# Kernel tuning notes

Hardware: AMD Instinct MI355X
Metric: run time of the kernel (lower is better)

The kernel has to match this reference:

```python
import jax, jax.numpy as jnp
import numpy as np

B, T, H, NH, L, V, FF = 2, 1024, 1024, 16, 6, 8192, 4096
D = H // NH
EPS = 1e-5


def _ln(x, g, b):
    mu = jnp.mean(x, axis=-1, keepdims=True)
    var = jnp.mean(jnp.square(x - mu), axis=-1, keepdims=True)
    return (x - mu) * jax.lax.rsqrt(var + EPS) * g + b


def setup_inputs() -> dict:
    key = jax.random.key(0)
    ks = jax.random.split(key, 12)
    s = 1.0 / np.sqrt(H)
    return {
        "x": jax.random.randint(ks[0], (B, T), 0, V),
        "tok_emb": jax.random.normal(ks[1], (V, H), jnp.float32) * s,
        "pos_emb": jax.random.normal(ks[2], (1, T, H), jnp.float32) * s,
        "Wq": jax.random.normal(ks[3], (L, H, H), jnp.float32) * s,
        "bq": jnp.zeros((L, H), jnp.float32),
        "Wk": jax.random.normal(ks[4], (L, H, H), jnp.float32) * s,
        "bk": jnp.zeros((L, H), jnp.float32),
        "Wv": jax.random.normal(ks[5], (L, H, H), jnp.float32) * s,
        "bv": jnp.zeros((L, H), jnp.float32),
        "Wo": jax.random.normal(ks[6], (L, H, H), jnp.float32) * s,
        "bo": jnp.zeros((L, H), jnp.float32),
        "W1": jax.random.normal(ks[7], (L, H, FF), jnp.float32) * s,
        "b1": jnp.zeros((L, FF), jnp.float32),
        "W2": jax.random.normal(ks[8], (L, FF, H), jnp.float32) * (1.0 / np.sqrt(FF)),
        "b2": jnp.zeros((L, H), jnp.float32),
        "ln1_g": jnp.ones((L, H), jnp.float32),
        "ln1_b": jnp.zeros((L, H), jnp.float32),
        "ln2_g": jnp.ones((L, H), jnp.float32),
        "ln2_b": jnp.zeros((L, H), jnp.float32),
        "lnf_g": jnp.ones((H,), jnp.float32),
        "lnf_b": jnp.zeros((H,), jnp.float32),
        "headW": jax.random.normal(ks[9], (H, V), jnp.float32) * s,
        "headb": jnp.zeros((V,), jnp.float32),
    }


def _transformer(x, tok_emb, pos_emb, Wq, bq, Wk, bk, Wv, bv, Wo, bo,
                 W1, b1, W2, b2, ln1_g, ln1_b, ln2_g, ln2_b, lnf_g, lnf_b,
                 headW, headb):
    Tcur = x.shape[1]
    h = tok_emb[x] + pos_emb[:, :Tcur, :]            # [B,T,H]
    mask = jnp.tril(jnp.ones((Tcur, Tcur), bool))    # causal [T,T]
    scale = 1.0 / np.sqrt(D)

    def block(h, p):
        (wq, q_b, wk, k_b, wv, v_b, wo, o_b,
         w1, b1_, w2, b2_, g1, be1, g2, be2) = p
        q = (h @ wq + q_b).reshape(B, Tcur, NH, D)
        k = (h @ wk + k_b).reshape(B, Tcur, NH, D)
        v = (h @ wv + v_b).reshape(B, Tcur, NH, D)
        att = jnp.einsum('bqnd,bknd->bnqk', q, k) * scale
        att = jnp.where(mask, att, -jnp.inf)
        w = jax.nn.softmax(att, axis=-1)
        o = jnp.einsum('bnqk,bknd->bqnd', w, v).reshape(B, Tcur, H)
        h = _ln(h + (o @ wo + o_b), g1, be1)          # post-LN after attention
        m = jax.nn.gelu(h @ w1 + b1_, approximate=False) @ w2 + b2_
        h = _ln(h + m, g2, be2)                       # post-LN after MLP
        return h, None

    params = (Wq, bq, Wk, bk, Wv, bv, Wo, bo, W1, b1, W2, b2,
              ln1_g, ln1_b, ln2_g, ln2_b)
    h, _ = jax.lax.scan(block, h, params)
    h = _ln(h, lnf_g, lnf_b)
    return h @ headW + headb                          # [B,T,V]


def reference(x, tok_emb, pos_emb, Wq, bq, Wk, bk, Wv, bv, Wo, bo,
              W1, b1, W2, b2, ln1_g, ln1_b, ln2_g, ln2_b, lnf_g, lnf_b,
              headW, headb):
    return _transformer(x, tok_emb, pos_emb, Wq, bq, Wk, bk, Wv, bv, Wo, bo,
                        W1, b1, W2, b2, ln1_g, ln1_b, ln2_g, ln2_b,
                        lnf_g, lnf_b, headW, headb)
```

## Files before the change

### kernel.cpp

```cpp
#include <hip/hip_runtime.h>
#include <hip/hip_bf16.h>

#define DEV __device__ __forceinline__

typedef unsigned short u16;
typedef __attribute__((ext_vector_type(8))) short bf16x8;
typedef __attribute__((ext_vector_type(4))) float f32x4;

static constexpr int MB_ = 2;
static constexpr int T_  = 1024;
static constexpr int H_  = 1024;
static constexpr int NH_ = 16;
static constexpr int L_  = 6;
static constexpr int V_  = 8192;
static constexpr int FF_ = 4096;
static constexpr int M_  = MB_ * T_;
static constexpr int QKVN = 3 * H_;

DEV u16 f2bf(float x) {
  __hip_bfloat16 h = __float2bfloat16(x);
  return *reinterpret_cast<u16*>(&h);
}

__global__ __launch_bounds__(256) void embed_kernel(
    const int* __restrict__ x, const float* __restrict__ tok,
    const float* __restrict__ pos, float* __restrict__ h, u16* __restrict__ hb)
{
  int i = blockIdx.x;
  int t = threadIdx.x;
  int id = x[i];
  int tt = i & (T_ - 1);
  float4 a = *(const float4*)(tok + (size_t)id * H_ + t * 4);
  float4 b = *(const float4*)(pos + (size_t)tt * H_ + t * 4);
  float4 r = make_float4(a.x + b.x, a.y + b.y, a.z + b.z, a.w + b.w);
  *(float4*)(h + (size_t)i * H_ + t * 4) = r;
  ushort4 u = make_ushort4(f2bf(r.x), f2bf(r.y), f2bf(r.z), f2bf(r.w));
  *(ushort4*)(hb + (size_t)i * H_ + t * 4) = u;
}

DEV void transpose_tile128(const float* __restrict__ W, u16* __restrict__ WT,
                           int R, int C, int bx, int by)
{
  __shared__ float Ts[64][65];
  const int t = threadIdx.x;
  const int lr = t >> 4;
  const int lcq = (t & 15) * 4;
  #pragma unroll
  for (int si = 0; si < 2; ++si) {
    #pragma unroll
    for (int sj = 0; sj < 2; ++sj) {
      const int r0 = by * 128 + si * 64, c0 = bx * 128 + sj * 64;
      #pragma unroll
      for (int it = 0; it < 4; ++it) {
        int r = it * 16 + lr;
        float4 v = *(const float4*)(W + (size_t)(r0 + r) * C + c0 + lcq);
        Ts[r][lcq + 0] = v.x; Ts[r][lcq + 1] = v.y;
        Ts[r][lcq + 2] = v.z; Ts[r][lcq + 3] = v.w;
      }
      __syncthreads();
      #pragma unroll
      for (int it = 0; it < 4; ++it) {
        int n = it * 16 + lr;
        ushort4 u = make_ushort4(f2bf(Ts[lcq + 0][n]), f2bf(Ts[lcq + 1][n]),
                                 f2bf(Ts[lcq + 2][n]), f2bf(Ts[lcq + 3][n]));
        *(ushort4*)(WT + (size_t)(c0 + n) * R + r0 + lcq) = u;
      }
      __syncthreads();
    }
  }
}

__global__ __launch_bounds__(256) void transpose_layer_k(
    const float* __restrict__ Wq, const float* __restrict__ Wk,
    const float* __restrict__ Wv, const float* __restrict__ Wo,
    const float* __restrict__ W1, const float* __restrict__ W2,
    u16* qkvT, u16* oT, u16* w1T, u16* w2T)
{
  int t = blockIdx.x;
  if (t < 256) {
    int m = t >> 6, idx = t & 63, bx = idx & 7, by = idx >> 3;
    const float* W = (m == 0) ? Wq : (m == 1) ? Wk : (m == 2) ? Wv : Wo;
    u16* WT = (m == 3) ? oT : qkvT + (size_t)m * H_ * H_;
    transpose_tile128(W, WT, H_, H_, bx, by);
  } else if (t < 512) {
    int idx = t - 256;
    transpose_tile128(W1, w1T, H_, FF_, idx & 31, idx >> 5);
  } else {
    int idx = t - 512;
    transpose_tile128(W2, w2T, FF_, H_, idx & 7, idx >> 3);
  }
}

__global__ __launch_bounds__(256) void transpose_head_k(
    const float* __restrict__ hW, u16* __restrict__ hT)
{
  int idx = blockIdx.x;
  transpose_tile128(hW, hT, H_, V_, idx & 63, idx >> 6);
}

__global__ __launch_bounds__(256) void concat_qkv_bias(
    const float* __restrict__ bq, const float* __restrict__ bk,
    const float* __restrict__ bv, float* __restrict__ outb)
{
  int l = blockIdx.x;
  for (int j = threadIdx.x; j < H_; j += 256) {
    outb[(size_t)l * QKVN + j]          = bq[(size_t)l * H_ + j];
    outb[(size_t)l * QKVN + H_ + j]     = bk[(size_t)l * H_ + j];
    outb[(size_t)l * QKVN + 2 * H_ + j] = bv[(size_t)l * H_ + j];
  }
}


#define GLOAD_LDS16(g, l)                                              \
  __builtin_amdgcn_global_load_lds(                                    \
      (const __attribute__((address_space(1))) void*)(g),              \
      (__attribute__((address_space(3))) void*)(l), 16, 0, 0)

DEV void stage_t(const u16* __restrict__ G, int ldk, int r0g, int kofs,
                 u16* lds, int w, int lane)
{
  const int rl = ((lane >> 3) << 1) | ((lane >> 2) & 1);
  #pragma unroll
  for (int j = 0; j < 2; ++j) {
    const int row0 = w * 32 + j * 16;
    const int row = row0 + rl;
    const int c = (lane & 3) ^ (((row0 >> 1) + (lane >> 3)) & 3);
    const u16* g = G + (size_t)(r0g + row) * ldk + kofs + c * 8;
    GLOAD_LDS16(g, lds + row0 * 32);
  }
}

DEV bf16x8 frag3(const u16* lds, int rr, int ch) {
  return *(const bf16x8*)(lds + (rr >> 1) * 64 + (rr & 1) * 32 +
                          ((ch ^ ((rr >> 1) & 3)) * 8));
}

template<int N>
DEV void wait_vm_barrier() {
  asm volatile("s_waitcnt vmcnt(%0)" :: "n"(N) : "memory");
  __builtin_amdgcn_s_barrier();
}

DEV void comp3(const u16* As, const u16* Bs, f32x4 (&acc)[4][4],
               int wr, int wc, int lc, int lg)
{
  bf16x8 af[4], bv[4];
  #pragma unroll
  for (int mi = 0; mi < 4; ++mi)
    af[mi] = frag3(As, wr * 64 + mi * 16 + lc, lg);
  #pragma unroll
  for (int ni = 0; ni < 4; ++ni)
    bv[ni] = frag3(Bs, wc * 64 + ni * 16 + lc, lg);
  #pragma unroll
  for (int mi = 0; mi < 4; ++mi)
    #pragma unroll
    for (int ni = 0; ni < 4; ++ni)
      acc[mi][ni] = __builtin_amdgcn_mfma_f32_16x16x32_bf16(af[mi], bv[ni], acc[mi][ni], 0, 0, 0);
}

template<bool PARTIAL, bool DO_GELU, bool WF, bool WB>
__global__ __launch_bounds__(256, 2) void gemm3(
    const u16* __restrict__ A, const u16* __restrict__ BT,
    const float* __restrict__ bias, float* __restrict__ Cf,
    u16* __restrict__ Cb, float* __restrict__ P, int N, int K, int Ksub)
{
  __shared__ __align__(16) u16 As[4][128][32];
  __shared__ __align__(16) u16 Bs[4][128][32];

  const int tid = threadIdx.x;
  const int lane = tid & 63, w = tid >> 6;
  const int wr = w >> 1, wc = w & 1;
  const int lc = lane & 15, lg = lane >> 4;

  const int gx = gridDim.x, gy = gridDim.y;
  const int nwg = gx * gy;
  const int lid = blockIdx.y * gx + blockIdx.x;
  const int q8 = nwg >> 3, r8s = nwg & 7;
  const int xcd = lid & 7, ord = lid >> 3;
  const int sid = (xcd < r8s ? xcd * (q8 + 1) : r8s * (q8 + 1) + (xcd - r8s) * q8) + ord;
  const int m0 = (sid % gy) * 128, n0 = (sid / gy) * 128;

  const int kb = blockIdx.z * Ksub;
  const int NT = Ksub >> 5;

  f32x4 acc[4][4];
  #pragma unroll
  for (int i = 0; i < 4; ++i)
    #pragma unroll
    for (int j = 0; j < 4; ++j) {
      f32x4 z = {0.f, 0.f, 0.f, 0.f};
      acc[i][j] = z;
    }

  auto STG = [&](int t, int b) {
    stage_t(A,  K, m0, kb + t * 32, &As[b][0][0], w, lane);
    stage_t(BT, K, n0, kb + t * 32, &Bs[b][0][0], w, lane);
  };

  STG(0, 0);
  STG(1, 1);
  int t = 0;
  for (; t < NT - 2; ++t) {
    STG(t + 2, (t + 2) & 3);
    wait_vm_barrier<8>();
    comp3(&As[t & 3][0][0], &Bs[t & 3][0][0], acc, wr, wc, lc, lg);
  }
  wait_vm_barrier<4>();
  comp3(&As[t & 3][0][0], &Bs[t & 3][0][0], acc, wr, wc, lc, lg);
  ++t;
  wait_vm_barrier<0>();
  comp3(&As[t & 3][0][0], &Bs[t & 3][0][0], acc, wr, wc, lc, lg);

  const size_t zofs = (size_t)blockIdx.z * M_ * N;
  #pragma unroll
  for (int mi = 0; mi < 4; ++mi) {
    #pragma unroll
    for (int ni = 0; ni < 4; ++ni) {
      int gn = n0 + wc * 64 + ni * 16 + lc;
      float bvv = PARTIAL ? 0.f : bias[gn];
      #pragma unroll
      for (int r = 0; r < 4; ++r) {
        int gm = m0 + wr * 64 + mi * 16 + lg * 4 + r;
        float v = acc[mi][ni][r];
        if (PARTIAL) {
          P[zofs + (size_t)gm * N + gn] = v;
        } else {
          v += bvv;
          if (DO_GELU) v = 0.5f * v * (1.f + erff(v * 0.70710678118654752f));
          if (WF) Cf[(size_t)gm * N + gn] = v;
          if (WB) Cb[(size_t)gm * N + gn] = f2bf(v);
        }
      }
    }
  }
}

__global__ __launch_bounds__(256) void ln_kernel(
    const float* __restrict__ X,
    const float* __restrict__ g, const float* __restrict__ be,
    u16* __restrict__ Hb)
{
  __shared__ float red[8];
  int row = blockIdx.x, t = threadIdx.x;
  int lane = t & 63, w = t >> 6;
  float4 v = *(const float4*)(X + (size_t)row * H_ + t * 4);
  float s = v.x + v.y + v.z + v.w;
  float q = v.x * v.x + v.y * v.y + v.z * v.z + v.w * v.w;
  #pragma unroll
  for (int o = 1; o < 64; o <<= 1) { s += __shfl_xor(s, o); q += __shfl_xor(q, o); }
  if (lane == 0) { red[w] = s; red[4 + w] = q; }
  __syncthreads();
  float S = red[0] + red[1] + red[2] + red[3];
  float Q = red[4] + red[5] + red[6] + red[7];
  float mu  = S * (1.f / H_);
  float var = Q * (1.f / H_) - mu * mu;
  float inv = rsqrtf(var + 1e-5f);
  float4 gv = *(const float4*)(g  + t * 4);
  float4 bv = *(const float4*)(be + t * 4);
  ushort4 u = make_ushort4(f2bf((v.x - mu) * inv * gv.x + bv.x),
                           f2bf((v.y - mu) * inv * gv.y + bv.y),
                           f2bf((v.z - mu) * inv * gv.z + bv.z),
                           f2bf((v.w - mu) * inv * gv.w + bv.w));
  *(ushort4*)(Hb + (size_t)row * H_ + t * 4) = u;
}

__global__ __launch_bounds__(256) void ln2_kernel(
    const float* __restrict__ P, int S,
    const float* __restrict__ bias,
    const float* __restrict__ g, const float* __restrict__ be,
    float* __restrict__ h, u16* __restrict__ hb)
{
  __shared__ float red[8];
  int row = blockIdx.x, t = threadIdx.x;
  int lane = t & 63, w = t >> 6;
  float4 v = *(const float4*)(h + (size_t)row * H_ + t * 4);
  float4 bb = *(const float4*)(bias + t * 4);
  v.x += bb.x; v.y += bb.y; v.z += bb.z; v.w += bb.w;
  for (int s0 = 0; s0 < S; ++s0) {
    float4 p = *(const float4*)(P + (size_t)s0 * M_ * H_ + (size_t)row * H_ + t * 4);
    v.x += p.x; v.y += p.y; v.z += p.z; v.w += p.w;
  }
  float s = v.x + v.y + v.z + v.w;
  float q = v.x * v.x + v.y * v.y + v.z * v.z + v.w * v.w;
  #pragma unroll
  for (int o = 1; o < 64; o <<= 1) { s += __shfl_xor(s, o); q += __shfl_xor(q, o); }
  if (lane == 0) { red[w] = s; red[4 + w] = q; }
  __syncthreads();
  float S1 = red[0] + red[1] + red[2] + red[3];
  float Q1 = red[4] + red[5] + red[6] + red[7];
  float mu  = S1 * (1.f / H_);
  float var = Q1 * (1.f / H_) - mu * mu;
  float inv = rsqrtf(var + 1e-5f);
  float4 gv = *(const float4*)(g  + t * 4);
  float4 bv = *(const float4*)(be + t * 4);
  float o0 = (v.x - mu) * inv * gv.x + bv.x;
  float o1 = (v.y - mu) * inv * gv.y + bv.y;
  float o2 = (v.z - mu) * inv * gv.z + bv.z;
  float o3 = (v.w - mu) * inv * gv.w + bv.w;
  *(float4*)(h + (size_t)row * H_ + t * 4) = make_float4(o0, o1, o2, o3);
  ushort4 u = make_ushort4(f2bf(o0), f2bf(o1), f2bf(o2), f2bf(o3));
  *(ushort4*)(hb + (size_t)row * H_ + t * 4) = u;
}

__global__ __launch_bounds__(256) void attn_kernel(
    const u16* __restrict__ qkv, u16* __restrict__ Og)
{
  __shared__ __align__(16) u16 Ks[2][64][72];
  __shared__ __align__(16) u16 Vs[2][64][72];
  __shared__ __align__(16) u16 QPs[4][16][72];

  const int qb = gridDim.x - 1 - blockIdx.x;
  const int bh = blockIdx.y;
  const int b = bh >> 4, hh = bh & 15;
  const int q0 = qb * 64;
  const size_t base  = ((size_t)b * T_) * QKVN + (size_t)hh * 64;
  const size_t baseO = ((size_t)b * T_) * H_ + (size_t)hh * 64;

  const int tid = threadIdx.x;
  const int lane = tid & 63, w = tid >> 6;
  const int lc = lane & 15, lg = lane >> 4;

  const int r8 = tid >> 3, d8 = (tid & 7) << 3;
  const int vk = tid & 31, vd = (tid >> 5) << 3;

  u16* Qflat = &QPs[0][0][0];

  bf16x8 kr[2], vr[2];
  #pragma unroll
  for (int i = 0; i < 2; ++i) {
    kr[i] = *(const bf16x8*)(qkv + base + H_ + (size_t)(i * 32 + r8) * QKVN + d8);
    vr[i] = *(const bf16x8*)(qkv + base + 2 * H_ + (size_t)(i * 32 + vk) * QKVN + vd);
  }
  #pragma unroll
  for (int i = 0; i < 2; ++i)
    *(bf16x8*)(Qflat + (size_t)(i * 32 + r8) * 72 + d8) =
      *(const bf16x8*)(qkv + base + (size_t)(q0 + i * 32 + r8) * QKVN + d8);
  #pragma unroll
  for (int i = 0; i < 2; ++i) {
    *(bf16x8*)&Ks[0][i * 32 + r8][d8] = kr[i];
    #pragma unroll
    for (int j = 0; j < 8; ++j) Vs[0][vd + j][i * 32 + vk] = ((const u16*)&vr[i])[j];
  }
  __syncthreads();
  bf16x8 aq0 = *(const bf16x8*)(Qflat + (size_t)(w * 16 + lc) * 72 + lg * 8);
  bf16x8 aq1 = *(const bf16x8*)(Qflat + (size_t)(w * 16 + lc) * 72 + 32 + lg * 8);

  float m_r[4], l_r[4];
  f32x4 oa[4];
  #pragma unroll
  for (int i = 0; i < 4; ++i) {
    m_r[i] = -1e30f; l_r[i] = 0.f;
    f32x4 z = {0.f, 0.f, 0.f, 0.f};
    oa[i] = z;
  }
  const float sc2 = 0.125f * 1.4426950408889634f;

  for (int kv = 0; kv <= qb; ++kv) {
    const int cur = kv & 1, nxt = cur ^ 1;
    if (kv < qb) {
      #pragma unroll
      for (int i = 0; i < 2; ++i) {
        kr[i] = *(const bf16x8*)(qkv + base + H_ + (size_t)((kv + 1) * 64 + i * 32 + r8) * QKVN + d8);
        vr[i] = *(const bf16x8*)(qkv + base + 2 * H_ + (size_t)((kv + 1) * 64 + i * 32 + vk) * QKVN + vd);
      }
    }

    f32x4 sfr[4];
    #pragma unroll
    for (int ni = 0; ni < 4; ++ni) { f32x4 z = {0.f,0.f,0.f,0.f}; sfr[ni] = z; }
    #pragma unroll
    for (int ni = 0; ni < 4; ++ni) {
      bf16x8 bk0 = *(const bf16x8*)&Ks[cur][ni * 16 + lc][lg * 8];
      bf16x8 bk1 = *(const bf16x8*)&Ks[cur][ni * 16 + lc][32 + lg * 8];
      sfr[ni] = __builtin_amdgcn_mfma_f32_16x16x32_bf16(aq0, bk0, sfr[ni], 0, 0, 0);
      sfr[ni] = __builtin_amdgcn_mfma_f32_16x16x32_bf16(aq1, bk1, sfr[ni], 0, 0, 0);
    }
    if (kv == qb) {
      #pragma unroll
      for (int ni = 0; ni < 4; ++ni)
        #pragma unroll
        for (int r = 0; r < 4; ++r)
          if (ni * 16 + lc > w * 16 + lg * 4 + r) sfr[ni][r] = -1e30f;
    }
    #pragma unroll
    for (int r = 0; r < 4; ++r) {
      float pm = fmaxf(fmaxf(sfr[0][r], sfr[1][r]), fmaxf(sfr[2][r], sfr[3][r]));
      pm = fmaxf(pm, __shfl_xor(pm, 1));
      pm = fmaxf(pm, __shfl_xor(pm, 2));
      pm = fmaxf(pm, __shfl_xor(pm, 4));
      pm = fmaxf(pm, __shfl_xor(pm, 8));
      float mn = fmaxf(m_r[r], pm);
      float al = exp2f(sc2 * (m_r[r] - mn));
      m_r[r] = mn; l_r[r] *= al;
      #pragma unroll
      for (int f = 0; f < 4; ++f) oa[f][r] *= al;
      float rs = 0.f;
      #pragma unroll
      for (int ni = 0; ni < 4; ++ni) {
        float p = exp2f(sc2 * (sfr[ni][r] - mn));
        sfr[ni][r] = p; rs += p;
      }
      rs += __shfl_xor(rs, 1); rs += __shfl_xor(rs, 2);
      rs += __shfl_xor(rs, 4); rs += __shfl_xor(rs, 8);
      l_r[r] += rs;
    }
    #pragma unroll
    for (int ni = 0; ni < 4; ++ni)
      #pragma unroll
      for (int r = 0; r < 4; ++r)
        QPs[w][lg * 4 + r][ni * 16 + lc] = f2bf(sfr[ni][r]);
    bf16x8 ap0 = *(const bf16x8*)&QPs[w][lc][lg * 8];
    bf16x8 ap1 = *(const bf16x8*)&QPs[w][lc][32 + lg * 8];
    #pragma unroll
    for (int f = 0; f < 4; ++f) {
      bf16x8 bv0 = *(const bf16x8*)&Vs[cur][f * 16 + lc][lg * 8];
      bf16x8 bv1 = *(const bf16x8*)&Vs[cur][f * 16 + lc][32 + lg * 8];
      oa[f] = __builtin_amdgcn_mfma_f32_16x16x32_bf16(ap0, bv0, oa[f], 0, 0, 0);
      oa[f] = __builtin_amdgcn_mfma_f32_16x16x32_bf16(ap1, bv1, oa[f], 0, 0, 0);
    }

    if (kv < qb) {
      #pragma unroll
      for (int i = 0; i < 2; ++i) {
        *(bf16x8*)&Ks[nxt][i * 32 + r8][d8] = kr[i];
        #pragma unroll
        for (int j = 0; j < 8; ++j) Vs[nxt][vd + j][i * 32 + vk] = ((const u16*)&vr[i])[j];
      }
      __syncthreads();
    }
  }

  #pragma unroll
  for (int r = 0; r < 4; ++r) {
    float inv = 1.f / l_r[r];
    int grow = q0 + w * 16 + lg * 4 + r;
    #pragma unroll
    for (int f = 0; f < 4; ++f)
      Og[baseO + (size_t)grow * H_ + f * 16 + lc] = f2bf(oa[f][r] * inv);
  }
}

extern "C" void kernel_launch(void* const* d_in, const int* in_sizes, int n_in,
                              void* d_out, int out_size, void* d_ws, size_t ws_size,
                              hipStream_t stream)
{
  const int*   x    = (const int*)  d_in[0];
  const float* tok  = (const float*)d_in[1];
  const float* pos  = (const float*)d_in[2];
  const float* Wq   = (const float*)d_in[3];
  const float* bq   = (const float*)d_in[4];
  const float* Wk   = (const float*)d_in[5];
  const float* bk   = (const float*)d_in[6];
  const float* Wv   = (const float*)d_in[7];
  const float* bv   = (const float*)d_in[8];
  const float* Wo   = (const float*)d_in[9];
  const float* bo   = (const float*)d_in[10];
  const float* W1   = (const float*)d_in[11];
  const float* b1   = (const float*)d_in[12];
  const float* W2   = (const float*)d_in[13];
  const float* b2   = (const float*)d_in[14];
  const float* g1   = (const float*)d_in[15];
  const float* be1  = (const float*)d_in[16];
  const float* g2   = (const float*)d_in[17];
  const float* be2  = (const float*)d_in[18];
  const float* gf   = (const float*)d_in[19];
  const float* bef  = (const float*)d_in[20];
  const float* hW   = (const float*)d_in[21];
  const float* hbias= (const float*)d_in[22];
  float* out = (float*)d_out;

  char* wsp = (char*)d_ws;
  size_t off = 0;
  auto alloc = [&](size_t bytes) -> void* {
    void* p = wsp + off;
    off += (bytes + 255) & ~(size_t)255;
    return p;
  };
  float* h    = (float*)alloc((size_t)M_ * H_ * 4);
  u16*   hb   = (u16*)  alloc((size_t)M_ * H_ * 2);
  u16*   qkv  = (u16*)  alloc((size_t)M_ * QKVN * 2);
  u16*   ob_  = (u16*)  alloc((size_t)M_ * H_ * 2);
  u16*   m1   = (u16*)  alloc((size_t)M_ * FF_ * 2);
  float* P    = (float*)alloc((size_t)4 * M_ * H_ * 4);
  u16*   hT   = (u16*)P;
  u16*   qkvT = (u16*)  alloc((size_t)QKVN * H_ * 2);
  u16*   oT   = (u16*)  alloc((size_t)H_ * H_ * 2);
  u16*   w1T  = (u16*)  alloc((size_t)H_ * FF_ * 2);
  u16*   w2T  = (u16*)  alloc((size_t)FF_ * H_ * 2);
  float* bqkv = (float*)alloc((size_t)L_ * QKVN * 4);
  (void)in_sizes; (void)n_in; (void)out_size; (void)ws_size;

  embed_kernel<<<M_, 256, 0, stream>>>(x, tok, pos, h, hb);
  concat_qkv_bias<<<L_, 256, 0, stream>>>(bq, bk, bv, bqkv);

  for (int l = 0; l < L_; ++l) {
    transpose_layer_k<<<768, 256, 0, stream>>>(
        Wq + (size_t)l * H_ * H_, Wk + (size_t)l * H_ * H_,
        Wv + (size_t)l * H_ * H_, Wo + (size_t)l * H_ * H_,
        W1 + (size_t)l * H_ * FF_, W2 + (size_t)l * FF_ * H_,
        qkvT, oT, w1T, w2T);
    gemm3<false, false, false, true><<<dim3(QKVN / 128, M_ / 128, 1), 256, 0, stream>>>(
        hb, qkvT, bqkv + (size_t)l * QKVN, nullptr, qkv, nullptr, QKVN, H_, H_);
    attn_kernel<<<dim3(T_ / 64, MB_ * NH_), 256, 0, stream>>>(qkv, ob_);
    gemm3<true, false, false, false><<<dim3(H_ / 128, M_ / 128, 2), 256, 0, stream>>>(
        ob_, oT, nullptr, nullptr, nullptr, P, H_, H_, H_ / 2);
    ln2_kernel<<<M_, 256, 0, stream>>>(P, 2, bo + l * H_, g1 + l * H_, be1 + l * H_, h, hb);
    gemm3<false, true, false, true><<<dim3(FF_ / 128, M_ / 128, 1), 256, 0, stream>>>(
        hb, w1T, b1 + (size_t)l * FF_, nullptr, m1, nullptr, FF_, H_, H_);
    gemm3<true, false, false, false><<<dim3(H_ / 128, M_ / 128, 4), 256, 0, stream>>>(
        m1, w2T, nullptr, nullptr, nullptr, P, H_, FF_, FF_ / 4);
    ln2_kernel<<<M_, 256, 0, stream>>>(P, 4, b2 + l * H_, g2 + l * H_, be2 + l * H_, h, hb);
  }

  ln_kernel<<<M_, 256, 0, stream>>>(h, gf, bef, hb);
  transpose_head_k<<<512, 256, 0, stream>>>(hW, hT);
  gemm3<false, false, true, false><<<dim3(V_ / 128, M_ / 128, 1), 256, 0, stream>>>(
      hb, hT, hbias, out, nullptr, nullptr, V_, H_, H_);
}
```

Before: 1.109 ms.

## Overlap next-layer weight transposes with W1 GEMM in a fused launch

```diff
diff --git a/kernel.cpp b/kernel.cpp
--- a/kernel.cpp
+++ b/kernel.cpp
@@ -22,26 +22,36 @@
   return *reinterpret_cast<u16*>(&h);
 }
 
-__global__ __launch_bounds__(256) void embed_kernel(
+__global__ __launch_bounds__(256) void embed_concat_kernel(
     const int* __restrict__ x, const float* __restrict__ tok,
-    const float* __restrict__ pos, float* __restrict__ h, u16* __restrict__ hb)
+    const float* __restrict__ pos, float* __restrict__ h, u16* __restrict__ hb,
+    const float* __restrict__ bq, const float* __restrict__ bk,
+    const float* __restrict__ bv, float* __restrict__ outb)
 {
   int i = blockIdx.x;
-  int t = threadIdx.x;
-  int id = x[i];
-  int tt = i & (T_ - 1);
-  float4 a = *(const float4*)(tok + (size_t)id * H_ + t * 4);
-  float4 b = *(const float4*)(pos + (size_t)tt * H_ + t * 4);
-  float4 r = make_float4(a.x + b.x, a.y + b.y, a.z + b.z, a.w + b.w);
-  *(float4*)(h + (size_t)i * H_ + t * 4) = r;
-  ushort4 u = make_ushort4(f2bf(r.x), f2bf(r.y), f2bf(r.z), f2bf(r.w));
-  *(ushort4*)(hb + (size_t)i * H_ + t * 4) = u;
-}
-
-DEV void transpose_tile128(const float* __restrict__ W, u16* __restrict__ WT,
-                           int R, int C, int bx, int by)
-{
-  __shared__ float Ts[64][65];
+  if (i < M_) {
+    int t = threadIdx.x;
+    int id = x[i];
+    int tt = i & (T_ - 1);
+    float4 a = *(const float4*)(tok + (size_t)id * H_ + t * 4);
+    float4 b = *(const float4*)(pos + (size_t)tt * H_ + t * 4);
+    float4 r = make_float4(a.x + b.x, a.y + b.y, a.z + b.z, a.w + b.w);
+    *(float4*)(h + (size_t)i * H_ + t * 4) = r;
+    ushort4 u = make_ushort4(f2bf(r.x), f2bf(r.y), f2bf(r.z), f2bf(r.w));
+    *(ushort4*)(hb + (size_t)i * H_ + t * 4) = u;
+  } else {
+    int l = i - M_;
+    for (int j = threadIdx.x; j < H_; j += 256) {
+      outb[(size_t)l * QKVN + j]          = bq[(size_t)l * H_ + j];
+      outb[(size_t)l * QKVN + H_ + j]     = bk[(size_t)l * H_ + j];
+      outb[(size_t)l * QKVN + 2 * H_ + j] = bv[(size_t)l * H_ + j];
+    }
+  }
+}
+
+DEV void transpose_tile128s(float (*Ts)[65], const float* __restrict__ W,
+                            u16* __restrict__ WT, int R, int C, int bx, int by)
+{
   const int t = threadIdx.x;
   const int lr = t >> 4;
   const int lcq = (t & 15) * 4;
@@ -70,44 +80,33 @@
   }
 }
 
+DEV void transpose_layer_body(float (*Ts)[65], int t,
+    const float* Wq, const float* Wk, const float* Wv, const float* Wo,
+    const float* W1, const float* W2,
+    u16* qkvT, u16* oT, u16* w1T, u16* w2T)
+{
+  if (t < 256) {
+    int m = t >> 6, idx = t & 63, bx = idx & 7, by = idx >> 3;
+    const float* W = (m == 0) ? Wq : (m == 1) ? Wk : (m == 2) ? Wv : Wo;
+    u16* WT = (m == 3) ? oT : qkvT + (size_t)m * H_ * H_;
+    transpose_tile128s(Ts, W, WT, H_, H_, bx, by);
+  } else if (t < 512) {
+    int idx = t - 256;
+    transpose_tile128s(Ts, W1, w1T, H_, FF_, idx & 31, idx >> 5);
+  } else {
+    int idx = t - 512;
+    transpose_tile128s(Ts, W2, w2T, FF_, H_, idx & 7, idx >> 3);
+  }
+}
+
 __global__ __launch_bounds__(256) void transpose_layer_k(
     const float* __restrict__ Wq, const float* __restrict__ Wk,
     const float* __restrict__ Wv, const float* __restrict__ Wo,
     const float* __restrict__ W1, const float* __restrict__ W2,
     u16* qkvT, u16* oT, u16* w1T, u16* w2T)
 {
-  int t = blockIdx.x;
-  if (t < 256) {
-    int m = t >> 6, idx = t & 63, bx = idx & 7, by = idx >> 3;
-    const float* W = (m == 0) ? Wq : (m == 1) ? Wk : (m == 2) ? Wv : Wo;
-    u16* WT = (m == 3) ? oT : qkvT + (size_t)m * H_ * H_;
-    transpose_tile128(W, WT, H_, H_, bx, by);
-  } else if (t < 512) {
-    int idx = t - 256;
-    transpose_tile128(W1, w1T, H_, FF_, idx & 31, idx >> 5);
-  } else {
-    int idx = t - 512;
-    transpose_tile128(W2, w2T, FF_, H_, idx & 7, idx >> 3);
-  }
-}
-
-__global__ __launch_bounds__(256) void transpose_head_k(
-    const float* __restrict__ hW, u16* __restrict__ hT)
-{
-  int idx = blockIdx.x;
-  transpose_tile128(hW, hT, H_, V_, idx & 63, idx >> 6);
-}
-
-__global__ __launch_bounds__(256) void concat_qkv_bias(
-    const float* __restrict__ bq, const float* __restrict__ bk,
-    const float* __restrict__ bv, float* __restrict__ outb)
-{
-  int l = blockIdx.x;
-  for (int j = threadIdx.x; j < H_; j += 256) {
-    outb[(size_t)l * QKVN + j]          = bq[(size_t)l * H_ + j];
-    outb[(size_t)l * QKVN + H_ + j]     = bk[(size_t)l * H_ + j];
-    outb[(size_t)l * QKVN + 2 * H_ + j] = bv[(size_t)l * H_ + j];
-  }
+  __shared__ float Ts[64][65];
+  transpose_layer_body(Ts, blockIdx.x, Wq, Wk, Wv, Wo, W1, W2, qkvT, oT, w1T, w2T);
 }
 
 
@@ -159,28 +158,24 @@
 }
 
 template<bool PARTIAL, bool DO_GELU, bool WF, bool WB>
-__global__ __launch_bounds__(256, 2) void gemm3(
+DEV void gemm_body(u16* SMEM,
     const u16* __restrict__ A, const u16* __restrict__ BT,
     const float* __restrict__ bias, float* __restrict__ Cf,
-    u16* __restrict__ Cb, float* __restrict__ P, int N, int K, int Ksub)
-{
-  __shared__ __align__(16) u16 As[4][128][32];
-  __shared__ __align__(16) u16 Bs[4][128][32];
-
+    u16* __restrict__ Cb, float* __restrict__ P,
+    int N, int K, int Ksub, int lid, int nwgx, int nwgy, int zid)
+{
   const int tid = threadIdx.x;
   const int lane = tid & 63, w = tid >> 6;
   const int wr = w >> 1, wc = w & 1;
   const int lc = lane & 15, lg = lane >> 4;
 
-  const int gx = gridDim.x, gy = gridDim.y;
-  const int nwg = gx * gy;
-  const int lid = blockIdx.y * gx + blockIdx.x;
+  const int nwg = nwgx * nwgy;
   const int q8 = nwg >> 3, r8s = nwg & 7;
   const int xcd = lid & 7, ord = lid >> 3;
   const int sid = (xcd < r8s ? xcd * (q8 + 1) : r8s * (q8 + 1) + (xcd - r8s) * q8) + ord;
-  const int m0 = (sid % gy) * 128, n0 = (sid / gy) * 128;
-
-  const int kb = blockIdx.z * Ksub;
+  const int m0 = (sid % nwgy) * 128, n0 = (sid / nwgy) * 128;
+
+  const int kb = zid * Ksub;
   const int NT = Ksub >> 5;
 
   f32x4 acc[4][4];
@@ -193,8 +188,8 @@
     }
 
   auto STG = [&](int t, int b) {
-    stage_t(A,  K, m0, kb + t * 32, &As[b][0][0], w, lane);
-    stage_t(BT, K, n0, kb + t * 32, &Bs[b][0][0], w, lane);
+    stage_t(A,  K, m0, kb + t * 32, SMEM + b * 4096, w, lane);
+    stage_t(BT, K, n0, kb + t * 32, SMEM + 16384 + b * 4096, w, lane);
   };
 
   STG(0, 0);
@@ -203,15 +198,15 @@
   for (; t < NT - 2; ++t) {
     STG(t + 2, (t + 2) & 3);
     wait_vm_barrier<8>();
-    comp3(&As[t & 3][0][0], &Bs[t & 3][0][0], acc, wr, wc, lc, lg);
+    comp3(SMEM + (t & 3) * 4096, SMEM + 16384 + (t & 3) * 4096, acc, wr, wc, lc, lg);
   }
   wait_vm_barrier<4>();
-  comp3(&As[t & 3][0][0], &Bs[t & 3][0][0], acc, wr, wc, lc, lg);
+  comp3(SMEM + (t & 3) * 4096, SMEM + 16384 + (t & 3) * 4096, acc, wr, wc, lc, lg);
   ++t;
   wait_vm_barrier<0>();
-  comp3(&As[t & 3][0][0], &Bs[t & 3][0][0], acc, wr, wc, lc, lg);
-
-  const size_t zofs = (size_t)blockIdx.z * M_ * N;
+  comp3(SMEM + (t & 3) * 4096, SMEM + 16384 + (t & 3) * 4096, acc, wr, wc, lc, lg);
+
+  const size_t zofs = (size_t)zid * M_ * N;
   #pragma unroll
   for (int mi = 0; mi < 4; ++mi) {
     #pragma unroll
@@ -232,6 +227,41 @@
         }
       }
     }
+  }
+}
+
+template<bool PARTIAL, bool DO_GELU, bool WF, bool WB>
+__global__ __launch_bounds__(256, 2) void gemm3(
+    const u16* __restrict__ A, const u16* __restrict__ BT,
+    const float* __restrict__ bias, float* __restrict__ Cf,
+    u16* __restrict__ Cb, float* __restrict__ P, int N, int K, int Ksub)
+{
+  __shared__ __align__(16) u16 SMEM[32768];
+  gemm_body<PARTIAL, DO_GELU, WF, WB>(SMEM, A, BT, bias, Cf, Cb, P, N, K, Ksub,
+      blockIdx.y * gridDim.x + blockIdx.x, gridDim.x, gridDim.y, blockIdx.z);
+}
+
+__global__ __launch_bounds__(256, 2) void gemmW1_fused(
+    const u16* __restrict__ A, const u16* __restrict__ w1T,
+    const float* __restrict__ bias, u16* __restrict__ m1,
+    const float* nWq, const float* nWk, const float* nWv, const float* nWo,
+    const float* nW1, const float* nW2,
+    u16* nqkvT, u16* noT, u16* nw1T, u16* nw2T,
+    const float* hW, u16* hT)
+{
+  __shared__ __align__(16) u16 SMEM[32768];
+  const int id = blockIdx.x;
+  if (id < 512) {
+    gemm_body<false, true, false, true>(SMEM, A, w1T, bias, nullptr, m1, nullptr,
+                                        FF_, H_, H_, id, 32, 16, 0);
+  } else if (nWq) {
+    float (*Ts)[65] = (float(*)[65])SMEM;
+    transpose_layer_body(Ts, id - 512, nWq, nWk, nWv, nWo, nW1, nW2,
+                         nqkvT, noT, nw1T, nw2T);
+  } else {
+    float (*Ts)[65] = (float(*)[65])SMEM;
+    int idx = id - 512;
+    transpose_tile128s(Ts, hW, hT, H_, V_, idx & 63, idx >> 6);
   }
 }
 
@@ -482,38 +512,49 @@
   u16*   ob_  = (u16*)  alloc((size_t)M_ * H_ * 2);
   u16*   m1   = (u16*)  alloc((size_t)M_ * FF_ * 2);
   float* P    = (float*)alloc((size_t)4 * M_ * H_ * 4);
-  u16*   hT   = (u16*)P;
+  u16*   hT   = (u16*)  alloc((size_t)V_ * H_ * 2);
   u16*   qkvT = (u16*)  alloc((size_t)QKVN * H_ * 2);
   u16*   oT   = (u16*)  alloc((size_t)H_ * H_ * 2);
-  u16*   w1T  = (u16*)  alloc((size_t)H_ * FF_ * 2);
-  u16*   w2T  = (u16*)  alloc((size_t)FF_ * H_ * 2);
+  u16*   w1Tb = (u16*)  alloc((size_t)2 * H_ * FF_ * 2);
+  u16*   w2Tb = (u16*)  alloc((size_t)2 * FF_ * H_ * 2);
   float* bqkv = (float*)alloc((size_t)L_ * QKVN * 4);
   (void)in_sizes; (void)n_in; (void)out_size; (void)ws_size;
 
-  embed_kernel<<<M_, 256, 0, stream>>>(x, tok, pos, h, hb);
-  concat_qkv_bias<<<L_, 256, 0, stream>>>(bq, bk, bv, bqkv);
+  auto w1T = [&](int l) { return w1Tb + (size_t)(l & 1) * H_ * FF_; };
+  auto w2T = [&](int l) { return w2Tb + (size_t)(l & 1) * FF_ * H_; };
+
+  embed_concat_kernel<<<M_ + L_, 256, 0, stream>>>(x, tok, pos, h, hb,
+                                                   bq, bk, bv, bqkv);
+  transpose_layer_k<<<768, 256, 0, stream>>>(
+      Wq, Wk, Wv, Wo, W1, W2, qkvT, oT, w1T(0), w2T(0));
 
   for (int l = 0; l < L_; ++l) {
-    transpose_layer_k<<<768, 256, 0, stream>>>(
-        Wq + (size_t)l * H_ * H_, Wk + (size_t)l * H_ * H_,
-        Wv + (size_t)l * H_ * H_, Wo + (size_t)l * H_ * H_,
-        W1 + (size_t)l * H_ * FF_, W2 + (size_t)l * FF_ * H_,
-        qkvT, oT, w1T, w2T);
     gemm3<false, false, false, true><<<dim3(QKVN / 128, M_ / 128, 1), 256, 0, stream>>>(
         hb, qkvT, bqkv + (size_t)l * QKVN, nullptr, qkv, nullptr, QKVN, H_, H_);
     attn_kernel<<<dim3(T_ / 64, MB_ * NH_), 256, 0, stream>>>(qkv, ob_);
-    gemm3<true, false, false, false><<<dim3(H_ / 128, M_ / 128, 2), 256, 0, stream>>>(
-        ob_, oT, nullptr, nullptr, nullptr, P, H_, H_, H_ / 2);
-    ln2_kernel<<<M_, 256, 0, stream>>>(P, 2, bo + l * H_, g1 + l * H_, be1 + l * H_, h, hb);
-    gemm3<false, true, false, true><<<dim3(FF_ / 128, M_ / 128, 1), 256, 0, stream>>>(
-        hb, w1T, b1 + (size_t)l * FF_, nullptr, m1, nullptr, FF_, H_, H_);
     gemm3<true, false, false, false><<<dim3(H_ / 128, M_ / 128, 4), 256, 0, stream>>>(
-        m1, w2T, nullptr, nullptr, nullptr, P, H_, FF_, FF_ / 4);
+        ob_, oT, nullptr, nullptr, nullptr, P, H_, H_, H_ / 4);
+    ln2_kernel<<<M_, 256, 0, stream>>>(P, 4, bo + l * H_, g1 + l * H_, be1 + l * H_, h, hb);
+    if (l + 1 < L_) {
+      int nl = l + 1;
+      gemmW1_fused<<<512 + 768, 256, 0, stream>>>(
+          hb, w1T(l), b1 + (size_t)l * FF_, m1,
+          Wq + (size_t)nl * H_ * H_, Wk + (size_t)nl * H_ * H_,
+          Wv + (size_t)nl * H_ * H_, Wo + (size_t)nl * H_ * H_,
+          W1 + (size_t)nl * H_ * FF_, W2 + (size_t)nl * FF_ * H_,
+          qkvT, oT, w1T(nl), w2T(nl), nullptr, nullptr);
+    } else {
+      gemmW1_fused<<<512 + 512, 256, 0, stream>>>(
+          hb, w1T(l), b1 + (size_t)l * FF_, m1,
+          nullptr, nullptr, nullptr, nullptr, nullptr, nullptr,
+          nullptr, nullptr, nullptr, nullptr, hW, hT);
+    }
+    gemm3<true, false, false, false><<<dim3(H_ / 128, M_ / 128, 4), 256, 0, stream>>>(
+        m1, w2T(l), nullptr, nullptr, nullptr, P, H_, FF_, FF_ / 4);
     ln2_kernel<<<M_, 256, 0, stream>>>(P, 4, b2 + l * H_, g2 + l * H_, be2 + l * H_, h, hb);
   }
 
   ln_kernel<<<M_, 256, 0, stream>>>(h, gf, bef, hb);
-  transpose_head_k<<<512, 256, 0, stream>>>(hW, hT);
   gemm3<false, false, true, false><<<dim3(V_ / 128, M_ / 128, 1), 256, 0, stream>>>(
       hb, hT, hbias, out, nullptr, nullptr, V_, H_, H_);
 }
```

Measured after the change: 1.061 ms. -4.3%, faster.
